# Kernel optimization log

Measured on AMD Instinct MI355X. Metric: run time of the kernel, lower is better.

Reference implementation:

```python
import jax, jax.numpy as jnp
import numpy as np

N = 100000
E = 1600000
IN, HID, OUT = 128, 256, 128


def setup_inputs() -> dict:
    key = jax.random.key(0)
    ks = jax.random.split(key, 8)
    x = jax.random.normal(ks[0], (N, IN), dtype=jnp.float32)
    edge_index = jax.random.randint(ks[1], (2, E), 0, N, dtype=jnp.int64)
    # PyG SAGEConv params: lin_l (neighbor aggr, with bias), lin_r (root, no bias)
    def glorot(k, shape):
        fan_in = shape[1]
        return jax.random.normal(k, shape, dtype=jnp.float32) / jnp.sqrt(jnp.float32(fan_in))
    W1l = glorot(ks[2], (HID, IN)); b1 = jnp.zeros((HID,), jnp.float32)
    W1r = glorot(ks[3], (HID, IN))
    W2l = glorot(ks[4], (OUT, HID)); b2 = jnp.zeros((OUT,), jnp.float32)
    W2r = glorot(ks[5], (OUT, HID))
    return {"x": x, "edge_index": edge_index, "W1l": W1l, "b1": b1,
            "W1r": W1r, "W2l": W2l, "b2": b2, "W2r": W2r}


def sage_conv(x, row, col, Wl, b, Wr, n_nodes):
    # mean-aggregate neighbor features x[row] at target nodes col
    msg = x[row]                                               # [E, d]
    s = jax.ops.segment_sum(msg, col, num_segments=n_nodes)    # [N, d]
    deg = jax.ops.segment_sum(jnp.ones((row.shape[0], 1), x.dtype), col,
                              num_segments=n_nodes)            # [N, 1]
    mean = s / jnp.maximum(deg, 1.0)
    return mean @ Wl.T + b + x @ Wr.T


def reference(x, edge_index, W1l, b1, W1r, W2l, b2, W2r):
    row, col = edge_index[0], edge_index[1]
    h = sage_conv(x, row, col, W1l, b1, W1r, N)
    h = jax.nn.relu(h)
    # dropout is identity in eval mode
    out = sage_conv(h, row, col, W2l, b2, W2r, N)
    return out
```

## Files before the change

kernel.cpp:

```cpp
#include <hip/hip_runtime.h>
#include <hip/hip_bf16.h>
#include <hip/hip_fp16.h>

#define NN 100000
#define NE 1600000
#define NCHUNK ((NN + 127) / 128)
#define NPB 512
#define NB 256
#define CHUNK 8192
#define NCH ((NE + CHUNK - 1) / CHUNK)

typedef __attribute__((ext_vector_type(8))) short short8;
typedef __attribute__((ext_vector_type(4))) float float4v;
typedef __attribute__((ext_vector_type(2))) float float2v;

__device__ __forceinline__ unsigned short f2bf(float f) {
    unsigned int b = __float_as_uint(f);
    return (unsigned short)((b + 0x7fffu + ((b >> 16) & 1u)) >> 16);
}
__device__ __forceinline__ unsigned int pack_bf16(float lo, float hi) {
    return (unsigned int)f2bf(lo) | ((unsigned int)f2bf(hi) << 16);
}
__device__ __forceinline__ unsigned char f2fp8(float v) {
    int r = __builtin_amdgcn_cvt_pk_fp8_f32(v, v, 0, false);
    return (unsigned char)(r & 0xff);
}
__device__ __forceinline__ unsigned short pack2fp8(float lo, float hi) {
    int r = __builtin_amdgcn_cvt_pk_fp8_f32(lo, hi, 0, false);
    return (unsigned short)(r & 0xffff);
}
__device__ __forceinline__ float h2f(unsigned short u) {
    return __half2float(__ushort_as_half(u));
}

__global__ void k_prep(const float* x, const float* W1l, const float* W1r,
                       const float* W2l, const float* W2r, const int* ei,
                       unsigned int* axb_u, unsigned short* xf8, unsigned short* wb1,
                       unsigned short* wb2, int* bcnt, unsigned short* gz) {
    __shared__ int hh[NB];
    int b = blockIdx.x, t = threadIdx.x;
    if (b < 3125) {
#pragma unroll
        for (int k = 0; k < 8; k++) {
            int tt = b * 2048 + k * 256 + t;
            int node = tt >> 6, i = tt & 63;
            float2 v = ((const float2*)x)[tt];
            axb_u[(size_t)node * 128 + 64 + i] = pack_bf16(v.x, v.y);
            xf8[(size_t)node * 64 + i] = pack2fp8(v.x, v.y);
        }
    } else if (b < 3253) {
        int i = (b - 3125) * 256 + t;
        int r1 = i >> 7, c1 = i & 127;
        wb1[r1 * 256 + c1]       = f2bf(W1l[i]);
        wb1[r1 * 256 + 128 + c1] = f2bf(W1r[i]);
        wb2[i]         = f2bf(W2l[i]);
        wb2[32768 + i] = f2bf(W2r[i]);
    } else if (b < 3509) {
        hh[t] = 0;
        __syncthreads();
        int e0 = (b - 3253) * 6250;
        for (int e = e0 + t; e < e0 + 6250; e += 256)
            atomicAdd(&hh[ei[NE + e] >> 9], 1);
        __syncthreads();
        if (hh[t]) atomicAdd(&bcnt[t], hh[t]);
    } else {
        if (t < 64) xf8[(size_t)NN * 64 + t] = 0;
        else if (t < 128 && gz) gz[(size_t)NN * 64 + (t - 64)] = 0;
    }
}

__global__ void k_bscan(const int* bcnt, int* boff, int* bcur) {
    __shared__ int s[NB];
    int t = threadIdx.x;
    int v = bcnt[t];
    s[t] = v;
    __syncthreads();
    for (int d = 1; d < NB; d <<= 1) {
        int val = (t >= d) ? s[t - d] : 0;
        __syncthreads();
        s[t] += val;
        __syncthreads();
    }
    boff[t + 1] = s[t];
    if (t == 0) boff[0] = 0;
    bcur[t] = s[t] - v;
}

__global__ __launch_bounds__(256) void k_bscatter(const int* ei, int* bcur, unsigned int* pairs) {
    __shared__ unsigned int buf[CHUNK];
    __shared__ int cnt[NB];
    __shared__ int lbase[NB];
    __shared__ int lcur[NB];
    __shared__ int gpos[NB];
    int t = threadIdx.x;
    int e0 = blockIdx.x * CHUNK;
    int nedge = NE - e0; if (nedge > CHUNK) nedge = CHUNK;
    cnt[t] = 0;
    __syncthreads();
    for (int i = t; i < nedge; i += 256)
        atomicAdd(&cnt[ei[NE + e0 + i] >> 9], 1);
    __syncthreads();
    int v = cnt[t];
    lcur[t] = v;
    __syncthreads();
    for (int d = 1; d < NB; d <<= 1) {
        int val = (t >= d) ? lcur[t - d] : 0;
        __syncthreads();
        lcur[t] += val;
        __syncthreads();
    }
    lbase[t] = lcur[t] - v;
    gpos[t] = atomicAdd(&bcur[t], v);
    __syncthreads();
    lcur[t] = lbase[t];
    __syncthreads();
    for (int i = t; i < nedge; i += 256) {
        int r = ei[e0 + i], c = ei[NE + e0 + i];
        int b = c >> 9;
        int p = atomicAdd(&lcur[b], 1);
        buf[p] = (unsigned)r | ((unsigned)(c & 511) << 17);
    }
    __syncthreads();
    int wv = t >> 6, lane = t & 63;
    for (int b = wv; b < NB; b += 4) {
        int n = cnt[b], lb = lbase[b], gp = gpos[b];
        for (int i = lane; i < n; i += 64)
            pairs[gp + i] = buf[lb + i];
    }
}

__global__ __launch_bounds__(256) void k_build(const unsigned int* pairs, const int* boff,
                                               int* off, int* deg, int* csr, int* csr32) {
    __shared__ int ldeg[NPB];
    __shared__ int lcur[NPB];
    __shared__ int lini[NPB];
    __shared__ int sscan[256];
    int b = blockIdx.x;
    int nbase = b * NPB;
    if (nbase >= NN) return;
    int t = threadIdx.x;
    int base = boff[b], cntb = boff[b + 1] - base;
    ldeg[t] = 0; ldeg[t + 256] = 0;
    __syncthreads();
    for (int i = t; i < cntb; i += 256) {
        unsigned int pr = pairs[base + i];
        atomicAdd(&ldeg[pr >> 17], 1);
    }
    __syncthreads();
    int d0 = ldeg[2 * t], d1 = ldeg[2 * t + 1];
    int v = d0 + d1;
    sscan[t] = v;
    __syncthreads();
    for (int d = 1; d < 256; d <<= 1) {
        int val = (t >= d) ? sscan[t - d] : 0;
        __syncthreads();
        sscan[t] += val;
        __syncthreads();
    }
    int ex = sscan[t] - v;
    lcur[2 * t] = ex;      lcur[2 * t + 1] = ex + d0;
    lini[2 * t] = ex;      lini[2 * t + 1] = ex + d0;
    __syncthreads();
    int nloc = NN - nbase; if (nloc > NPB) nloc = NPB;
    for (int ln = t; ln < nloc; ln += 256) {
        off[nbase + ln] = base + lcur[ln];
        deg[nbase + ln] = ldeg[ln];
    }
    __syncthreads();
    if (csr32) {
        for (int ln = t; ln < nloc; ln += 256) {
            int dd = ldeg[ln];
            if (dd < 32) {
                int dq = (dd + 7) & ~7;
                for (int rk = dd; rk < dq; rk++)
                    csr32[(size_t)(nbase + ln) * 32 + rk] = NN;
            }
        }
        for (int i = t; i < cntb; i += 256) {
            unsigned int pr = pairs[base + i];
            int nd = pr >> 17;
            int p = atomicAdd(&lcur[nd], 1);
            int src = (int)(pr & 0x1FFFFu);
            csr[base + p] = src;
            int rk = p - lini[nd];
            if (rk < 32) csr32[(size_t)(nbase + nd) * 32 + rk] = src;
        }
    } else {
        for (int i = t; i < cntb; i += 256) {
            unsigned int pr = pairs[base + i];
            int p = atomicAdd(&lcur[pr >> 17], 1);
            csr[base + p] = (int)(pr & 0x1FFFFu);
        }
    }
}

__global__ __launch_bounds__(512) void k_agg1(const unsigned short* xf8, const int* off,
                                              const int* deg, const int* csr, const int* csr32,
                                              unsigned int* axb_w) {
    int wid = (blockIdx.x * 512 + threadIdx.x) >> 6;
    if (wid >= NN) return;
    int widu = __builtin_amdgcn_readfirstlane(wid);
    int lane = threadIdx.x & 63;
    int d = deg[widu];
    float a0 = 0.f, a1 = 0.f;
    if (csr32) {
        const int* c32 = csr32 + (size_t)widu * 32;
        int dm = d < 32 ? d : 32;
        int dq = (dm + 7) & ~7;
        for (int c = 0; c < dq; c += 8) {
#pragma unroll
            for (int r = 0; r < 8; r++) {
                int idx = c32[c + r];
                unsigned short u = xf8[(size_t)idx * 64 + lane];
                float2v f = __builtin_amdgcn_cvt_pk_f32_fp8((unsigned int)u, false);
                a0 += f.x; a1 += f.y;
            }
        }
        if (d > 32) {
            int start = off[widu];
            for (int j = 32; j < d; j++) {
                int idx = csr[start + j];
                unsigned short u = xf8[(size_t)idx * 64 + lane];
                float2v f = __builtin_amdgcn_cvt_pk_f32_fp8((unsigned int)u, false);
                a0 += f.x; a1 += f.y;
            }
        }
    } else {
        int start = off[widu];
        for (int j = 0; j < d; j++) {
            int idx = csr[start + j];
            unsigned short u = xf8[(size_t)idx * 64 + lane];
            float2v f = __builtin_amdgcn_cvt_pk_f32_fp8((unsigned int)u, false);
            a0 += f.x; a1 += f.y;
        }
    }
    float inv = 1.0f / (float)(d > 0 ? d : 1);
    axb_w[(size_t)wid * 128 + lane] = pack_bf16(a0 * inv, a1 * inv);
}

__global__ __launch_bounds__(512) void k_agg2(const unsigned short* g, const int* off,
                                              const int* deg, const int* csr, const int* csr32,
                                              const unsigned short* partial, float* out) {
    int wid = (blockIdx.x * 512 + threadIdx.x) >> 6;
    if (wid >= NN) return;
    int widu = __builtin_amdgcn_readfirstlane(wid);
    int lane = threadIdx.x & 63;
    int d = deg[widu];
    unsigned int pu = *(const unsigned int*)(partial + (size_t)widu * 128 + (lane << 1));
    float a0 = 0.f, a1 = 0.f;
    if (csr32) {
        const int* c32 = csr32 + (size_t)widu * 32;
        int dm = d < 32 ? d : 32;
        int dq = (dm + 7) & ~7;
        for (int c = 0; c < dq; c += 8) {
#pragma unroll
            for (int r = 0; r < 8; r++) {
                int idx = c32[c + r];
                unsigned short u = g[(size_t)idx * 64 + lane];
                float2v f = __builtin_amdgcn_cvt_pk_f32_fp8((unsigned int)u, false);
                a0 += f.x; a1 += f.y;
            }
        }
        if (d > 32) {
            int start = off[widu];
            for (int j = 32; j < d; j++) {
                int idx = csr[start + j];
                unsigned short u = g[(size_t)idx * 64 + lane];
                float2v f = __builtin_amdgcn_cvt_pk_f32_fp8((unsigned int)u, false);
                a0 += f.x; a1 += f.y;
            }
        }
    } else {
        int start = off[widu];
        for (int j = 0; j < d; j++) {
            int idx = csr[start + j];
            unsigned short u = g[(size_t)idx * 64 + lane];
            float2v f = __builtin_amdgcn_cvt_pk_f32_fp8((unsigned int)u, false);
            a0 += f.x; a1 += f.y;
        }
    }
    float inv = 1.0f / (float)(d > 0 ? d : 1);
    float2 o;
    o.x = h2f((unsigned short)(pu & 0xffff)) + a0 * inv;
    o.y = h2f((unsigned short)(pu >> 16)) + a1 * inv;
    *(float2*)(out + (size_t)wid * 128 + (lane << 1)) = o;
}

#define BROW 264
#define GGRID (32 * ((NCHUNK + 7) / 8))
__global__ __launch_bounds__(256, 4) void k_gemm1(const unsigned short* A, const unsigned short* wb,
                                                  const float* b1, unsigned short* H) {
    __shared__ unsigned short Bs[64 * BROW];
    int t = threadIdx.x;
    int b = blockIdx.x;
    int chunk = (b & 7) + ((b >> 5) << 3);
    int cg = (b >> 3) & 3;
    if (chunk >= NCHUNK) return;
    {
        const short8* src = (const short8*)(wb + (size_t)cg * 64 * 256);
        short8* dst = (short8*)Bs;
#pragma unroll
        for (int i = 0; i < 8; i++) {
            int gi = i * 256 + t;
            int r = gi >> 5, c = gi & 31;
            dst[r * 33 + c] = src[gi];
        }
    }
    __syncthreads();
    int wv = t >> 6, lane = t & 63;
    int mrow = lane & 15, quad = lane >> 4;
    int base = chunk * 128 + wv * 32;
    if (base >= NN) return;
    float bias[4];
#pragma unroll
    for (int ctl = 0; ctl < 4; ctl++) bias[ctl] = b1[cg * 64 + ctl * 16 + mrow];
    float4v acc[2][4];
#pragma unroll
    for (int h = 0; h < 2; h++)
#pragma unroll
        for (int ctl = 0; ctl < 4; ctl++) acc[h][ctl] = (float4v)(0.0f);
    const short8* a0p = (const short8*)(A + (size_t)(base + mrow) * 256);
    const short8* a1p = (const short8*)(A + (size_t)(base + 16 + mrow) * 256);
#pragma unroll
    for (int kk = 0; kk < 8; kk++) {
        short8 a0 = a0p[kk * 4 + quad];
        short8 a1 = a1p[kk * 4 + quad];
        int koff = kk * 32 + quad * 8;
#pragma unroll
        for (int ctl = 0; ctl < 4; ctl++) {
            short8 bfr = *(const short8*)(Bs + (ctl * 16 + mrow) * BROW + koff);
            acc[0][ctl] = __builtin_amdgcn_mfma_f32_16x16x32_bf16(a0, bfr, acc[0][ctl], 0, 0, 0);
            acc[1][ctl] = __builtin_amdgcn_mfma_f32_16x16x32_bf16(a1, bfr, acc[1][ctl], 0, 0, 0);
        }
    }
#pragma unroll
    for (int ctl = 0; ctl < 4; ctl++) {
        int col = cg * 64 + ctl * 16 + mrow;
#pragma unroll
        for (int h = 0; h < 2; h++)
#pragma unroll
            for (int r = 0; r < 4; r++) {
                int node = base + h * 16 + quad * 4 + r;
                float v = acc[h][ctl][r] + bias[ctl];
                H[(size_t)node * 256 + col] = f2bf(fmaxf(v, 0.f));
            }
    }
}

__global__ __launch_bounds__(256, 4) void k_gemm2(const unsigned short* A, const unsigned short* wb,
                                                  const float* b2, unsigned char* g,
                                                  unsigned short* partial) {
    __shared__ unsigned short Bs[64 * BROW];
    int t = threadIdx.x;
    int b = blockIdx.x;
    int chunk = (b & 7) + ((b >> 5) << 3);
    int cg = (b >> 3) & 3;
    if (chunk >= NCHUNK) return;
    {
        const short8* src = (const short8*)(wb + (size_t)cg * 64 * 256);
        short8* dst = (short8*)Bs;
#pragma unroll
        for (int i = 0; i < 8; i++) {
            int gi = i * 256 + t;
            int r = gi >> 5, c = gi & 31;
            dst[r * 33 + c] = src[gi];
        }
    }
    __syncthreads();
    int wv = t >> 6, lane = t & 63;
    int mrow = lane & 15, quad = lane >> 4;
    int base = chunk * 128 + wv * 32;
    if (base >= NN) return;
    float bias[4];
#pragma unroll
    for (int ctl = 0; ctl < 4; ctl++)
        bias[ctl] = (cg >= 2) ? b2[cg * 64 + ctl * 16 + mrow - 128] : 0.f;
    float4v acc[2][4];
#pragma unroll
    for (int h = 0; h < 2; h++)
#pragma unroll
        for (int ctl = 0; ctl < 4; ctl++) acc[h][ctl] = (float4v)(0.0f);
    const short8* a0p = (const short8*)(A + (size_t)(base + mrow) * 256);
    const short8* a1p = (const short8*)(A + (size_t)(base + 16 + mrow) * 256);
#pragma unroll
    for (int kk = 0; kk < 8; kk++) {
        short8 a0 = a0p[kk * 4 + quad];
        short8 a1 = a1p[kk * 4 + quad];
        int koff = kk * 32 + quad * 8;
#pragma unroll
        for (int ctl = 0; ctl < 4; ctl++) {
            short8 bfr = *(const short8*)(Bs + (ctl * 16 + mrow) * BROW + koff);
            acc[0][ctl] = __builtin_amdgcn_mfma_f32_16x16x32_bf16(a0, bfr, acc[0][ctl], 0, 0, 0);
            acc[1][ctl] = __builtin_amdgcn_mfma_f32_16x16x32_bf16(a1, bfr, acc[1][ctl], 0, 0, 0);
        }
    }
    if (cg < 2) {
#pragma unroll
        for (int ctl = 0; ctl < 4; ctl++) {
            int col = cg * 64 + ctl * 16 + mrow;
#pragma unroll
            for (int h = 0; h < 2; h++)
#pragma unroll
                for (int r = 0; r < 4; r++) {
                    int node = base + h * 16 + quad * 4 + r;
                    g[(size_t)node * 128 + col] = f2fp8(acc[h][ctl][r]);
                }
        }
    } else {
#pragma unroll
        for (int ctl = 0; ctl < 4; ctl++) {
            int pcol = cg * 64 + ctl * 16 + mrow - 128;
#pragma unroll
            for (int h = 0; h < 2; h++)
#pragma unroll
                for (int r = 0; r < 4; r++) {
                    int node = base + h * 16 + quad * 4 + r;
                    __half hf = __float2half(acc[h][ctl][r] + bias[ctl]);
                    partial[(size_t)node * 128 + pcol] = __half_as_ushort(hf);
                }
        }
    }
}

extern "C" void kernel_launch(void* const* d_in, const int* in_sizes, int n_in,
                              void* d_out, int out_size, void* d_ws, size_t ws_size,
                              hipStream_t stream) {
    const float* x   = (const float*)d_in[0];
    const int*   ei  = (const int*)d_in[1];
    const float* W1l = (const float*)d_in[2];
    const float* b1  = (const float*)d_in[3];
    const float* W1r = (const float*)d_in[4];
    const float* W2l = (const float*)d_in[5];
    const float* b2  = (const float*)d_in[6];
    const float* W2r = (const float*)d_in[7];
    float* out = (float*)d_out;

    char* p = (char*)d_ws;
    unsigned int* axb = (unsigned int*)p; p += (size_t)NN * 256 * 2;
    unsigned short* h = (unsigned short*)p; p += (size_t)NN * 256 * 2;
    unsigned char* g  = (unsigned char*)p; p += (size_t)NN * 128 + 256;
    unsigned short* xf8 = (unsigned short*)p; p += (size_t)NN * 128 + 256;
    unsigned short* wb1 = (unsigned short*)p; p += 65536 * 2;
    unsigned short* wb2 = (unsigned short*)p; p += 65536 * 2;
    int* deg  = (int*)p; p += (size_t)NN * 4;
    int* off  = (int*)p; p += (size_t)NN * 4;
    int* csr  = (int*)p; p += (size_t)NE * 4;
    int* bcnt = (int*)p; p += NB * 4;
    int* boff = (int*)p; p += (NB + 1) * 4;
    int* bcur = (int*)p; p += NB * 4;
    if (ws_size < (size_t)(p - (char*)d_ws)) return;
    int* csr32 = (int*)p; p += (size_t)NN * 32 * 4;
    if (ws_size < (size_t)(p - (char*)d_ws)) csr32 = nullptr;
    unsigned int* pairs = (unsigned int*)h;
    unsigned short* partial = (unsigned short*)axb;

    hipMemsetAsync(bcnt, 0, NB * 4, stream);
    k_prep<<<3510, 256, 0, stream>>>(x, W1l, W1r, W2l, W2r, ei, axb, xf8, wb1, wb2, bcnt,
                                     (unsigned short*)g);
    k_bscan<<<1, NB, 0, stream>>>(bcnt, boff, bcur);
    k_bscatter<<<NCH, 256, 0, stream>>>(ei, bcur, pairs);
    k_build<<<NB, 256, 0, stream>>>(pairs, boff, off, deg, csr, csr32);
    k_agg1<<<12500, 512, 0, stream>>>(xf8, off, deg, csr, csr32, axb);
    k_gemm1<<<GGRID, 256, 0, stream>>>((const unsigned short*)axb, wb1, b1, h);
    k_gemm2<<<GGRID, 256, 0, stream>>>(h, wb2, b2, g, partial);
    k_agg2<<<12500, 512, 0, stream>>>((const unsigned short*)g, off, deg, csr, csr32, partial, out);
}
```

Measured before the change: 361.1 us.

## Fuse both GEMM layers into one kernel keeping hidden activations in LDS

Merges the two GEMM kernels into one. Each block computes a 128-node tile of the first layer (bias plus ReLU), stores the bf16 hidden tile in shared memory, then runs the second-layer GEMM from LDS. This removes the global write and re-read of the N×256 hidden tensor and one kernel launch. In exchange, B fragments are now read straight from global/L2 instead of staged in LDS, a large LDS tile limits occupancy to 2 blocks, and the grid shrinks to one block per chunk, lowering parallelism.

```diff
diff --git a/kernel.cpp b/kernel.cpp
--- a/kernel.cpp
+++ b/kernel.cpp
@@ -286,138 +286,114 @@
     *(float2*)(out + (size_t)wid * 128 + (lane << 1)) = o;
 }
 
-#define BROW 264
-#define GGRID (32 * ((NCHUNK + 7) / 8))
-__global__ __launch_bounds__(256, 4) void k_gemm1(const unsigned short* A, const unsigned short* wb,
-                                                  const float* b1, unsigned short* H) {
-    __shared__ unsigned short Bs[64 * BROW];
+#define HROW 264
+__global__ __launch_bounds__(256, 2) void k_gemmf(const unsigned short* A,
+                                                  const unsigned short* wb1,
+                                                  const unsigned short* wb2,
+                                                  const float* b1, const float* b2,
+                                                  unsigned char* g, unsigned short* partial) {
+    __shared__ unsigned short Hs[128 * HROW];
     int t = threadIdx.x;
-    int b = blockIdx.x;
-    int chunk = (b & 7) + ((b >> 5) << 3);
-    int cg = (b >> 3) & 3;
-    if (chunk >= NCHUNK) return;
-    {
-        const short8* src = (const short8*)(wb + (size_t)cg * 64 * 256);
-        short8* dst = (short8*)Bs;
-#pragma unroll
-        for (int i = 0; i < 8; i++) {
-            int gi = i * 256 + t;
-            int r = gi >> 5, c = gi & 31;
-            dst[r * 33 + c] = src[gi];
-        }
-    }
-    __syncthreads();
-    int wv = t >> 6, lane = t & 63;
+    int cg = t >> 6;
+    int lane = t & 63;
     int mrow = lane & 15, quad = lane >> 4;
-    int base = chunk * 128 + wv * 32;
-    if (base >= NN) return;
-    float bias[4];
-#pragma unroll
-    for (int ctl = 0; ctl < 4; ctl++) bias[ctl] = b1[cg * 64 + ctl * 16 + mrow];
-    float4v acc[2][4];
-#pragma unroll
-    for (int h = 0; h < 2; h++)
-#pragma unroll
-        for (int ctl = 0; ctl < 4; ctl++) acc[h][ctl] = (float4v)(0.0f);
-    const short8* a0p = (const short8*)(A + (size_t)(base + mrow) * 256);
-    const short8* a1p = (const short8*)(A + (size_t)(base + 16 + mrow) * 256);
-#pragma unroll
-    for (int kk = 0; kk < 8; kk++) {
-        short8 a0 = a0p[kk * 4 + quad];
-        short8 a1 = a1p[kk * 4 + quad];
-        int koff = kk * 32 + quad * 8;
-#pragma unroll
-        for (int ctl = 0; ctl < 4; ctl++) {
-            short8 bfr = *(const short8*)(Bs + (ctl * 16 + mrow) * BROW + koff);
-            acc[0][ctl] = __builtin_amdgcn_mfma_f32_16x16x32_bf16(a0, bfr, acc[0][ctl], 0, 0, 0);
-            acc[1][ctl] = __builtin_amdgcn_mfma_f32_16x16x32_bf16(a1, bfr, acc[1][ctl], 0, 0, 0);
-        }
-    }
-#pragma unroll
-    for (int ctl = 0; ctl < 4; ctl++) {
-        int col = cg * 64 + ctl * 16 + mrow;
-#pragma unroll
-        for (int h = 0; h < 2; h++)
-#pragma unroll
-            for (int r = 0; r < 4; r++) {
-                int node = base + h * 16 + quad * 4 + r;
-                float v = acc[h][ctl][r] + bias[ctl];
-                H[(size_t)node * 256 + col] = f2bf(fmaxf(v, 0.f));
-            }
-    }
-}
-
-__global__ __launch_bounds__(256, 4) void k_gemm2(const unsigned short* A, const unsigned short* wb,
-                                                  const float* b2, unsigned char* g,
-                                                  unsigned short* partial) {
-    __shared__ unsigned short Bs[64 * BROW];
-    int t = threadIdx.x;
-    int b = blockIdx.x;
-    int chunk = (b & 7) + ((b >> 5) << 3);
-    int cg = (b >> 3) & 3;
-    if (chunk >= NCHUNK) return;
-    {
-        const short8* src = (const short8*)(wb + (size_t)cg * 64 * 256);
-        short8* dst = (short8*)Bs;
-#pragma unroll
-        for (int i = 0; i < 8; i++) {
-            int gi = i * 256 + t;
-            int r = gi >> 5, c = gi & 31;
-            dst[r * 33 + c] = src[gi];
-        }
-    }
-    __syncthreads();
-    int wv = t >> 6, lane = t & 63;
-    int mrow = lane & 15, quad = lane >> 4;
-    int base = chunk * 128 + wv * 32;
-    if (base >= NN) return;
-    float bias[4];
-#pragma unroll
-    for (int ctl = 0; ctl < 4; ctl++)
-        bias[ctl] = (cg >= 2) ? b2[cg * 64 + ctl * 16 + mrow - 128] : 0.f;
-    float4v acc[2][4];
-#pragma unroll
-    for (int h = 0; h < 2; h++)
-#pragma unroll
-        for (int ctl = 0; ctl < 4; ctl++) acc[h][ctl] = (float4v)(0.0f);
-    const short8* a0p = (const short8*)(A + (size_t)(base + mrow) * 256);
-    const short8* a1p = (const short8*)(A + (size_t)(base + 16 + mrow) * 256);
-#pragma unroll
-    for (int kk = 0; kk < 8; kk++) {
-        short8 a0 = a0p[kk * 4 + quad];
-        short8 a1 = a1p[kk * 4 + quad];
-        int koff = kk * 32 + quad * 8;
-#pragma unroll
-        for (int ctl = 0; ctl < 4; ctl++) {
-            short8 bfr = *(const short8*)(Bs + (ctl * 16 + mrow) * BROW + koff);
-            acc[0][ctl] = __builtin_amdgcn_mfma_f32_16x16x32_bf16(a0, bfr, acc[0][ctl], 0, 0, 0);
-            acc[1][ctl] = __builtin_amdgcn_mfma_f32_16x16x32_bf16(a1, bfr, acc[1][ctl], 0, 0, 0);
-        }
-    }
-    if (cg < 2) {
-#pragma unroll
-        for (int ctl = 0; ctl < 4; ctl++) {
-            int col = cg * 64 + ctl * 16 + mrow;
-#pragma unroll
-            for (int h = 0; h < 2; h++)
+    int base = blockIdx.x * 128;
+    int koff = quad * 8;
+
+    float bias1[4];
+#pragma unroll
+    for (int ct = 0; ct < 4; ct++) bias1[ct] = b1[cg * 64 + ct * 16 + mrow];
+#pragma unroll
+    for (int half = 0; half < 2; half++) {
+        float4v acc[4][4];
+#pragma unroll
+        for (int h = 0; h < 4; h++)
+#pragma unroll
+            for (int ct = 0; ct < 4; ct++) acc[h][ct] = (float4v)(0.0f);
+#pragma unroll
+        for (int kk = 0; kk < 8; kk++) {
+            short8 af[4];
+#pragma unroll
+            for (int h = 0; h < 4; h++)
+                af[h] = *(const short8*)(A + (size_t)(base + half * 64 + h * 16 + mrow) * 256
+                                         + kk * 32 + koff);
+#pragma unroll
+            for (int ct = 0; ct < 4; ct++) {
+                short8 bf = *(const short8*)(wb1 + (size_t)(cg * 64 + ct * 16 + mrow) * 256
+                                             + kk * 32 + koff);
+#pragma unroll
+                for (int h = 0; h < 4; h++)
+                    acc[h][ct] = __builtin_amdgcn_mfma_f32_16x16x32_bf16(af[h], bf, acc[h][ct], 0, 0, 0);
+            }
+        }
+#pragma unroll
+        for (int ct = 0; ct < 4; ct++) {
+            int col = cg * 64 + ct * 16 + mrow;
+#pragma unroll
+            for (int h = 0; h < 4; h++)
 #pragma unroll
                 for (int r = 0; r < 4; r++) {
-                    int node = base + h * 16 + quad * 4 + r;
-                    g[(size_t)node * 128 + col] = f2fp8(acc[h][ctl][r]);
+                    int nrow = half * 64 + h * 16 + quad * 4 + r;
+                    Hs[nrow * HROW + col] = f2bf(fmaxf(acc[h][ct][r] + bias1[ct], 0.f));
                 }
         }
-    } else {
-#pragma unroll
-        for (int ctl = 0; ctl < 4; ctl++) {
-            int pcol = cg * 64 + ctl * 16 + mrow - 128;
-#pragma unroll
-            for (int h = 0; h < 2; h++)
-#pragma unroll
-                for (int r = 0; r < 4; r++) {
-                    int node = base + h * 16 + quad * 4 + r;
-                    __half hf = __float2half(acc[h][ctl][r] + bias[ctl]);
-                    partial[(size_t)node * 128 + pcol] = __half_as_ushort(hf);
-                }
+    }
+    __syncthreads();
+
+    float bias2[4];
+#pragma unroll
+    for (int ct = 0; ct < 4; ct++)
+        bias2[ct] = (cg >= 2) ? b2[(cg - 2) * 64 + ct * 16 + mrow] : 0.f;
+#pragma unroll
+    for (int half = 0; half < 2; half++) {
+        float4v acc[4][4];
+#pragma unroll
+        for (int h = 0; h < 4; h++)
+#pragma unroll
+            for (int ct = 0; ct < 4; ct++) acc[h][ct] = (float4v)(0.0f);
+#pragma unroll
+        for (int kk = 0; kk < 8; kk++) {
+            short8 af[4];
+#pragma unroll
+            for (int h = 0; h < 4; h++)
+                af[h] = *(const short8*)(Hs + (half * 64 + h * 16 + mrow) * HROW + kk * 32 + koff);
+#pragma unroll
+            for (int ct = 0; ct < 4; ct++) {
+                short8 bf = *(const short8*)(wb2 + (size_t)(cg * 64 + ct * 16 + mrow) * 256
+                                             + kk * 32 + koff);
+#pragma unroll
+                for (int h = 0; h < 4; h++)
+                    acc[h][ct] = __builtin_amdgcn_mfma_f32_16x16x32_bf16(af[h], bf, acc[h][ct], 0, 0, 0);
+            }
+        }
+        if (cg < 2) {
+#pragma unroll
+            for (int ct = 0; ct < 4; ct++) {
+                int col = cg * 64 + ct * 16 + mrow;
+#pragma unroll
+                for (int h = 0; h < 4; h++)
+#pragma unroll
+                    for (int r = 0; r < 4; r++) {
+                        int node = base + half * 64 + h * 16 + quad * 4 + r;
+                        if (node < NN)
+                            g[(size_t)node * 128 + col] = f2fp8(acc[h][ct][r]);
+                    }
+            }
+        } else {
+#pragma unroll
+            for (int ct = 0; ct < 4; ct++) {
+                int pcol = (cg - 2) * 64 + ct * 16 + mrow;
+#pragma unroll
+                for (int h = 0; h < 4; h++)
+#pragma unroll
+                    for (int r = 0; r < 4; r++) {
+                        int node = base + half * 64 + h * 16 + quad * 4 + r;
+                        if (node < NN) {
+                            __half hf = __float2half(acc[h][ct][r] + bias2[ct]);
+                            partial[(size_t)node * 128 + pcol] = __half_as_ushort(hf);
+                        }
+                    }
+            }
         }
     }
 }
@@ -452,7 +428,7 @@
     int* csr32 = (int*)p; p += (size_t)NN * 32 * 4;
     if (ws_size < (size_t)(p - (char*)d_ws)) csr32 = nullptr;
     unsigned int* pairs = (unsigned int*)h;
-    unsigned short* partial = (unsigned short*)axb;
+    unsigned short* partial = h + (size_t)NN * 128;
 
     hipMemsetAsync(bcnt, 0, NB * 4, stream);
     k_prep<<<3510, 256, 0, stream>>>(x, W1l, W1r, W2l, W2r, ei, axb, xf8, wb1, wb2, bcnt,
@@ -461,7 +437,6 @@
     k_bscatter<<<NCH, 256, 0, stream>>>(ei, bcur, pairs);
     k_build<<<NB, 256, 0, stream>>>(pairs, boff, off, deg, csr, csr32);
     k_agg1<<<12500, 512, 0, stream>>>(xf8, off, deg, csr, csr32, axb);
-    k_gemm1<<<GGRID, 256, 0, stream>>>((const unsigned short*)axb, wb1, b1, h);
-    k_gemm2<<<GGRID, 256, 0, stream>>>(h, wb2, b2, g, partial);
+    k_gemmf<<<NCHUNK, 256, 0, stream>>>((const unsigned short*)axb, wb1, wb2, b1, b2, g, partial);
     k_agg2<<<12500, 512, 0, stream>>>((const unsigned short*)g, off, deg, csr, csr32, partial, out);
 }
```

New measurement: 386.6 us. 7.1% more time.
